# Performance work log

Hardware: AMD Instinct MI355X
Metric: run time of the kernel (lower is better)

Reference implementation:

```python
import jax, jax.numpy as jnp
import numpy as np

N, E, IN, H, OUT = 50000, 800000, 128, 128, 64
BN_EPS = 1e-5


def setup_inputs() -> dict:
    key = jax.random.key(0)
    ks = jax.random.split(key, 12)
    x = jax.random.normal(ks[0], (N, IN), dtype=jnp.float32)
    edge_index = jax.random.randint(ks[1], (2, E), 0, N, dtype=jnp.int32)
    def lin(k, fan_in, fan_out):
        s = 1.0 / np.sqrt(fan_in)
        return jax.random.uniform(k, (fan_in, fan_out), jnp.float32, -s, s)
    params = {
        'W1': lin(ks[2], IN, H),  'b1': jnp.zeros((H,), jnp.float32),
        'W2': lin(ks[3], H, H),   'b2': jnp.zeros((H,), jnp.float32),
        'W3': lin(ks[4], H, H),   'b3': jnp.zeros((H,), jnp.float32),
        'W4': lin(ks[5], H, OUT), 'b4': jnp.zeros((OUT,), jnp.float32),
        'g1': jnp.ones((H,), jnp.float32), 'be1': jnp.zeros((H,), jnp.float32),
        'g2': jnp.ones((H,), jnp.float32), 'be2': jnp.zeros((H,), jnp.float32),
        'g3': jnp.ones((H,), jnp.float32), 'be3': jnp.zeros((H,), jnp.float32),
    }
    return dict(x=x, edge_index=edge_index, **params)


def _gcn_conv(x, src, dst, dinv, norm, W, b):
    # GCNConv: symmetric-normalized aggregation with self loops.
    h = x @ W                                   # [N, F]
    agg = jax.ops.segment_sum(h[src] * norm[:, None], dst, num_segments=N)
    agg = agg + h * (dinv * dinv)[:, None]      # self-loop contribution
    return agg + b


def _bn(x, gamma, beta):
    mu = jnp.mean(x, axis=0)
    var = jnp.mean(jnp.square(x - mu), axis=0)
    return (x - mu) * jax.lax.rsqrt(var + BN_EPS) * gamma + beta


def reference(x, edge_index, W1, b1, W2, b2, W3, b3, W4, b4, g1, be1, g2, be2, g3, be3):
    src, dst = edge_index[0], edge_index[1]
    # degree with self loops; fixed by the graph, shared across layers
    deg = jax.ops.segment_sum(jnp.ones((E,), x.dtype), dst, num_segments=N) + 1.0
    dinv = jax.lax.rsqrt(deg)
    norm = dinv[src] * dinv[dst]                # [E]

    h = _gcn_conv(x, src, dst, dinv, norm, W1, b1)
    h = jax.nn.relu(_bn(h, g1, be1))
    h = _gcn_conv(h, src, dst, dinv, norm, W2, b2)
    h = jax.nn.relu(_bn(h, g2, be2))
    h = _gcn_conv(h, src, dst, dinv, norm, W3, b3)
    h = jax.nn.relu(_bn(h, g3, be3))
    return _gcn_conv(h, src, dst, dinv, norm, W4, b4)
```

## Files before the change

kernel.cpp:

```cpp
#include <hip/hip_runtime.h>

constexpr int NN = 50000;
constexpr int NE = 800000;
constexpr float EPS = 1e-5f;

constexpr int CAP     = 64;
constexpr int FILL_NB = (NE + 255) / 256;
constexpr int WCONV_NB = (57344 + 255) / 256;
constexpr int GEMM1_NB = (NN + 63) / 64;

constexpr int GROUPS   = 197;
constexpr int FUSED_NB = GROUPS * 21;

typedef short bf16x8 __attribute__((ext_vector_type(8)));
typedef float f32x4  __attribute__((ext_vector_type(4)));

__device__ __forceinline__ ushort f2bf(float x) {
    union { float f; unsigned u; } a; a.f = x;
    unsigned u = a.u;
    unsigned r = (u + 0x7FFFu + ((u >> 16) & 1u)) >> 16;
    return (ushort)r;
}
__device__ __forceinline__ float bflo(unsigned p) {
    union { unsigned u; float f; } a; a.u = p << 16; return a.f;
}
__device__ __forceinline__ float bfhi(unsigned p) {
    union { unsigned u; float f; } a; a.u = p & 0xFFFF0000u; return a.f;
}

__global__ __launch_bounds__(256, 3) void fused_prep_gemm1(
    const int* __restrict__ src, const int* __restrict__ dst,
    int* __restrict__ curA, int* __restrict__ curB,
    ushort* __restrict__ csrf,
    const float* __restrict__ W1, const float* __restrict__ W2,
    const float* __restrict__ W3, const float* __restrict__ W4,
    ushort* __restrict__ Wt,
    const float* __restrict__ X, ushort* __restrict__ U)
{
    constexpr int LDK = 136;
    __shared__ __align__(16) ushort Xs[64 * LDK];

    const int bx  = blockIdx.x;
    const int g   = bx / 21;
    const int l   = bx - g * 21;
    const int tid = threadIdx.x;

    if (l >= 4) {
        int fid = g * 17 + (l - 4);
        if (fid < FILL_NB) {
            int e = fid * 256 + tid;
            if (e < NE) {
                int d = dst[e];
                if (e < NE / 2) {
                    int slot = atomicAdd(&curA[d], 1);
                    if (slot < CAP) csrf[(size_t)d * CAP + slot] = (ushort)src[e];
                } else {
                    int old = atomicAdd(&curB[d], 1);
                    int slot = CAP - 1 - old;
                    if (slot >= 0) csrf[(size_t)d * CAP + slot] = (ushort)src[e];
                }
            }
        } else {
            int id = (fid - FILL_NB) * 256 + tid;
            if (id < 49152) {
                int li = id / 16384, r = id % 16384;
                int n = r >> 7, k = r & 127;
                const float* W = (li == 0) ? W1 : (li == 1) ? W2 : W3;
                Wt[li * 16384 + n * 128 + k] = f2bf(W[k * 128 + n]);
            } else if (id < 57344) {
                int r = id - 49152;
                int n = r >> 7, k = r & 127;
                Wt[49152 + n * 128 + k] = f2bf(W4[k * 64 + n]);
            }
        }
        return;
    }

    int tile = g * 4 + l;
    if (tile >= GEMM1_NB) return;

    const int wave = tid >> 6;
    const int lane = tid & 63;
    const int m    = lane & 15;
    const int q    = lane >> 4;
    const int rowHalf = wave & 1;
    const int colHalf = wave >> 1;
    const int row0 = tile * 64;

    bf16x8 w[4][4];
#pragma unroll
    for (int nt = 0; nt < 4; nt++) {
#pragma unroll
        for (int ks = 0; ks < 4; ks++) {
            const float* wp = &W1[(ks * 32 + q * 8) * 128 + colHalf * 64 + nt * 16 + m];
            bf16x8 t;
#pragma unroll
            for (int j = 0; j < 8; j++) t[j] = (short)f2bf(wp[j * 128]);
            w[nt][ks] = t;
        }
    }

#pragma unroll
    for (int it = 0; it < 8; it++) {
        int idx = it * 256 + tid;
        int r   = idx >> 5;
        int c4  = (idx & 31) * 4;
        int row = row0 + r;
        float4 v = make_float4(0.f, 0.f, 0.f, 0.f);
        if (row < NN) v = *(const float4*)&X[(size_t)row * 128 + c4];
        ushort4 o;
        o.x = f2bf(v.x); o.y = f2bf(v.y); o.z = f2bf(v.z); o.w = f2bf(v.w);
        *(ushort4*)&Xs[r * LDK + c4] = o;
    }
    __syncthreads();

    f32x4 acc[2][4];
#pragma unroll
    for (int t = 0; t < 2; t++)
#pragma unroll
        for (int nt = 0; nt < 4; nt++) acc[t][nt] = (f32x4){0.f, 0.f, 0.f, 0.f};

#pragma unroll
    for (int ks = 0; ks < 4; ks++) {
        bf16x8 a0 = *(const bf16x8*)&Xs[(rowHalf * 32 + m)      * LDK + ks * 32 + q * 8];
        bf16x8 a1 = *(const bf16x8*)&Xs[(rowHalf * 32 + 16 + m) * LDK + ks * 32 + q * 8];
#pragma unroll
        for (int nt = 0; nt < 4; nt++) {
            acc[0][nt] = __builtin_amdgcn_mfma_f32_16x16x32_bf16(a0, w[nt][ks], acc[0][nt], 0, 0, 0);
            acc[1][nt] = __builtin_amdgcn_mfma_f32_16x16x32_bf16(a1, w[nt][ks], acc[1][nt], 0, 0, 0);
        }
    }

#pragma unroll
    for (int t = 0; t < 2; t++) {
#pragma unroll
        for (int r = 0; r < 4; r++) {
            int row = row0 + rowHalf * 32 + t * 16 + q * 4 + r;
            if (row < NN) {
#pragma unroll
                for (int nt = 0; nt < 4; nt++)
                    U[(size_t)row * 128 + colHalf * 64 + nt * 16 + m] = f2bf(acc[t][nt][r]);
            }
        }
    }
}

template<int F, bool BN>
__global__ __launch_bounds__(256, 3) void gemm_bf16_kernel(
    const void* __restrict__ Xv, const ushort* __restrict__ Wt,
    const int* __restrict__ curA, const int* __restrict__ curB,
    const float* __restrict__ sums, const float* __restrict__ sumsq,
    const float* __restrict__ g, const float* __restrict__ be,
    ushort* __restrict__ U)
{
    constexpr int NTW = F / 32;
    constexpr int LDK = 136;
    __shared__ __align__(16) ushort Xs[64 * LDK];
    __shared__ float scs[128], shs[128];

    const int tid  = threadIdx.x;
    const int wave = tid >> 6;
    const int lane = tid & 63;
    const int m    = lane & 15;
    const int q    = lane >> 4;
    const int rowHalf = wave & 1;
    const int colHalf = wave >> 1;
    const int row0 = blockIdx.x * 64;

    if constexpr (BN) {
        if (tid < 128) {
            float mu  = sums[tid] * (1.0f / NN);
            float var = sumsq[tid] * (1.0f / NN) - mu * mu;
            float scv = rsqrtf(var + EPS) * g[tid];
            scs[tid] = scv;
            shs[tid] = be[tid] - mu * scv;
        }
        __syncthreads();
    }

    bf16x8 w[NTW][4];
#pragma unroll
    for (int nt = 0; nt < NTW; nt++)
#pragma unroll
        for (int ks = 0; ks < 4; ks++)
            w[nt][ks] = *(const bf16x8*)&Wt[(colHalf * (F / 2) + nt * 16 + m) * 128 + ks * 32 + q * 8];

#pragma unroll
    for (int it = 0; it < 8; it++) {
        int idx = it * 256 + tid;
        int r   = idx >> 5;
        int c4  = (idx & 31) * 4;
        int row = row0 + r;
        float4 v = make_float4(0.f, 0.f, 0.f, 0.f);
        if constexpr (BN) {
            if (row < NN) {
                uint2 p = *(const uint2*)&((const ushort*)Xv)[(size_t)row * 128 + c4];
                v.x = bflo(p.x); v.y = bfhi(p.x);
                v.z = bflo(p.y); v.w = bfhi(p.y);
            }
            float4 s = *(const float4*)&scs[c4];
            float4 h = *(const float4*)&shs[c4];
            v.x = fmaxf(0.f, v.x * s.x + h.x);
            v.y = fmaxf(0.f, v.y * s.y + h.y);
            v.z = fmaxf(0.f, v.z * s.z + h.z);
            v.w = fmaxf(0.f, v.w * s.w + h.w);
        } else {
            if (row < NN) v = *(const float4*)&((const float*)Xv)[(size_t)row * 128 + c4];
        }
        ushort4 o;
        o.x = f2bf(v.x); o.y = f2bf(v.y); o.z = f2bf(v.z); o.w = f2bf(v.w);
        *(ushort4*)&Xs[r * LDK + c4] = o;
    }
    __syncthreads();

    f32x4 acc[2][NTW];
#pragma unroll
    for (int t = 0; t < 2; t++)
#pragma unroll
        for (int nt = 0; nt < NTW; nt++) acc[t][nt] = (f32x4){0.f, 0.f, 0.f, 0.f};

#pragma unroll
    for (int ks = 0; ks < 4; ks++) {
        bf16x8 a0 = *(const bf16x8*)&Xs[(rowHalf * 32 + m)      * LDK + ks * 32 + q * 8];
        bf16x8 a1 = *(const bf16x8*)&Xs[(rowHalf * 32 + 16 + m) * LDK + ks * 32 + q * 8];
#pragma unroll
        for (int nt = 0; nt < NTW; nt++) {
            acc[0][nt] = __builtin_amdgcn_mfma_f32_16x16x32_bf16(a0, w[nt][ks], acc[0][nt], 0, 0, 0);
            acc[1][nt] = __builtin_amdgcn_mfma_f32_16x16x32_bf16(a1, w[nt][ks], acc[1][nt], 0, 0, 0);
        }
    }

#pragma unroll
    for (int t = 0; t < 2; t++) {
#pragma unroll
        for (int r = 0; r < 4; r++) {
            int row = row0 + rowHalf * 32 + t * 16 + q * 4 + r;
            if (row < NN) {
                float di = rsqrtf((float)(curA[row] + curB[row]) + 1.0f);
#pragma unroll
                for (int nt = 0; nt < NTW; nt++) {
                    U[(size_t)row * F + colHalf * (F / 2) + nt * 16 + m] = f2bf(acc[t][nt][r] * di);
                }
            }
        }
    }
}

template<bool SRCSCALE>
__global__ __launch_bounds__(256) void gather128_kernel(
    const ushort* __restrict__ csrf,
    const int* __restrict__ curA, const int* __restrict__ curB,
    const ushort* __restrict__ U, const float* __restrict__ b,
    ushort* __restrict__ Yb)
{
    int n    = (blockIdx.x * 256 + threadIdx.x) >> 6;
    int lane = threadIdx.x & 63;
    if (n >= NN) return;
    const int half = lane >> 5;
    const int c4   = (lane & 31) * 4;
    int dA = curA[n], dB = curB[n];
    int degRaw = dA + dB;
    int dA_c = min(dA, CAP);
    int dB_c = min(dB, CAP - dA_c);
    const int cnt = dA_c + dB_c;
    const int gap = CAP - cnt;
    int myIdx = (int)csrf[(size_t)n * CAP + lane];
    float myDs = 0.f;
    if constexpr (SRCSCALE) {
        int mi = min(myIdx, NN - 1);
        myDs = rsqrtf((float)(curA[mi] + curB[mi]) + 1.0f);
    }
    float a0 = 0.f, a1 = 0.f, a2 = 0.f, a3 = 0.f;

#define GSLOT(v) ((v) < dA_c ? (v) : (v) + gap)

    int j = 0;
    for (; j + 16 <= cnt; j += 16) {
        int s0 = __shfl(myIdx, GSLOT(j + 0  + half));
        int s1 = __shfl(myIdx, GSLOT(j + 2  + half));
        int s2 = __shfl(myIdx, GSLOT(j + 4  + half));
        int s3 = __shfl(myIdx, GSLOT(j + 6  + half));
        int s4 = __shfl(myIdx, GSLOT(j + 8  + half));
        int s5 = __shfl(myIdx, GSLOT(j + 10 + half));
        int s6 = __shfl(myIdx, GSLOT(j + 12 + half));
        int s7 = __shfl(myIdx, GSLOT(j + 14 + half));
        uint2 u0 = *(const uint2*)&U[(size_t)s0 * 128 + c4];
        uint2 u1 = *(const uint2*)&U[(size_t)s1 * 128 + c4];
        uint2 u2 = *(const uint2*)&U[(size_t)s2 * 128 + c4];
        uint2 u3 = *(const uint2*)&U[(size_t)s3 * 128 + c4];
        uint2 u4 = *(const uint2*)&U[(size_t)s4 * 128 + c4];
        uint2 u5 = *(const uint2*)&U[(size_t)s5 * 128 + c4];
        uint2 u6 = *(const uint2*)&U[(size_t)s6 * 128 + c4];
        uint2 u7 = *(const uint2*)&U[(size_t)s7 * 128 + c4];
        if constexpr (SRCSCALE) {
            float c0 = __shfl(myDs, GSLOT(j + 0  + half));
            float c1 = __shfl(myDs, GSLOT(j + 2  + half));
            float c2 = __shfl(myDs, GSLOT(j + 4  + half));
            float c3 = __shfl(myDs, GSLOT(j + 6  + half));
            float c5 = __shfl(myDs, GSLOT(j + 10 + half));
            float c4s = __shfl(myDs, GSLOT(j + 8 + half));
            float c6 = __shfl(myDs, GSLOT(j + 12 + half));
            float c7 = __shfl(myDs, GSLOT(j + 14 + half));
            a0 += c0 * bflo(u0.x) + c1 * bflo(u1.x) + c2 * bflo(u2.x) + c3 * bflo(u3.x)
                + c4s * bflo(u4.x) + c5 * bflo(u5.x) + c6 * bflo(u6.x) + c7 * bflo(u7.x);
            a1 += c0 * bfhi(u0.x) + c1 * bfhi(u1.x) + c2 * bfhi(u2.x) + c3 * bfhi(u3.x)
                + c4s * bfhi(u4.x) + c5 * bfhi(u5.x) + c6 * bfhi(u6.x) + c7 * bfhi(u7.x);
            a2 += c0 * bflo(u0.y) + c1 * bflo(u1.y) + c2 * bflo(u2.y) + c3 * bflo(u3.y)
                + c4s * bflo(u4.y) + c5 * bflo(u5.y) + c6 * bflo(u6.y) + c7 * bflo(u7.y);
            a3 += c0 * bfhi(u0.y) + c1 * bfhi(u1.y) + c2 * bfhi(u2.y) + c3 * bfhi(u3.y)
                + c4s * bfhi(u4.y) + c5 * bfhi(u5.y) + c6 * bfhi(u6.y) + c7 * bfhi(u7.y);
        } else {
            a0 += bflo(u0.x) + bflo(u1.x) + bflo(u2.x) + bflo(u3.x)
                + bflo(u4.x) + bflo(u5.x) + bflo(u6.x) + bflo(u7.x);
            a1 += bfhi(u0.x) + bfhi(u1.x) + bfhi(u2.x) + bfhi(u3.x)
                + bfhi(u4.x) + bfhi(u5.x) + bfhi(u6.x) + bfhi(u7.x);
            a2 += bflo(u0.y) + bflo(u1.y) + bflo(u2.y) + bflo(u3.y)
                + bflo(u4.y) + bflo(u5.y) + bflo(u6.y) + bflo(u7.y);
            a3 += bfhi(u0.y) + bfhi(u1.y) + bfhi(u2.y) + bfhi(u3.y)
                + bfhi(u4.y) + bfhi(u5.y) + bfhi(u6.y) + bfhi(u7.y);
        }
    }
    for (; j + 8 <= cnt; j += 8) {
        int s0 = __shfl(myIdx, GSLOT(j + 0 + half));
        int s1 = __shfl(myIdx, GSLOT(j + 2 + half));
        int s2 = __shfl(myIdx, GSLOT(j + 4 + half));
        int s3 = __shfl(myIdx, GSLOT(j + 6 + half));
        uint2 u0 = *(const uint2*)&U[(size_t)s0 * 128 + c4];
        uint2 u1 = *(const uint2*)&U[(size_t)s1 * 128 + c4];
        uint2 u2 = *(const uint2*)&U[(size_t)s2 * 128 + c4];
        uint2 u3 = *(const uint2*)&U[(size_t)s3 * 128 + c4];
        if constexpr (SRCSCALE) {
            float c0 = __shfl(myDs, GSLOT(j + 0 + half));
            float c1 = __shfl(myDs, GSLOT(j + 2 + half));
            float c2 = __shfl(myDs, GSLOT(j + 4 + half));
            float c3 = __shfl(myDs, GSLOT(j + 6 + half));
            a0 += c0 * bflo(u0.x) + c1 * bflo(u1.x) + c2 * bflo(u2.x) + c3 * bflo(u3.x);
            a1 += c0 * bfhi(u0.x) + c1 * bfhi(u1.x) + c2 * bfhi(u2.x) + c3 * bfhi(u3.x);
            a2 += c0 * bflo(u0.y) + c1 * bflo(u1.y) + c2 * bflo(u2.y) + c3 * bflo(u3.y);
            a3 += c0 * bfhi(u0.y) + c1 * bfhi(u1.y) + c2 * bfhi(u2.y) + c3 * bfhi(u3.y);
        } else {
            a0 += bflo(u0.x) + bflo(u1.x) + bflo(u2.x) + bflo(u3.x);
            a1 += bfhi(u0.x) + bfhi(u1.x) + bfhi(u2.x) + bfhi(u3.x);
            a2 += bflo(u0.y) + bflo(u1.y) + bflo(u2.y) + bflo(u3.y);
            a3 += bfhi(u0.y) + bfhi(u1.y) + bfhi(u2.y) + bfhi(u3.y);
        }
    }
    for (; j + 4 <= cnt; j += 4) {
        int s0 = __shfl(myIdx, GSLOT(j + 0 + half));
        int s1 = __shfl(myIdx, GSLOT(j + 2 + half));
        uint2 u0 = *(const uint2*)&U[(size_t)s0 * 128 + c4];
        uint2 u1 = *(const uint2*)&U[(size_t)s1 * 128 + c4];
        if constexpr (SRCSCALE) {
            float c0 = __shfl(myDs, GSLOT(j + 0 + half));
            float c1 = __shfl(myDs, GSLOT(j + 2 + half));
            a0 += c0 * bflo(u0.x) + c1 * bflo(u1.x);
            a1 += c0 * bfhi(u0.x) + c1 * bfhi(u1.x);
            a2 += c0 * bflo(u0.y) + c1 * bflo(u1.y);
            a3 += c0 * bfhi(u0.y) + c1 * bfhi(u1.y);
        } else {
            a0 += bflo(u0.x) + bflo(u1.x);
            a1 += bfhi(u0.x) + bfhi(u1.x);
            a2 += bflo(u0.y) + bflo(u1.y);
            a3 += bfhi(u0.y) + bfhi(u1.y);
        }
    }
    for (; j < cnt; j += 2) {
        int jj = j + half;
        int vv = min(jj, cnt - 1);
        int sl = GSLOT(vv);
        int s  = __shfl(myIdx, sl);
        float sc = 1.f;
        if constexpr (SRCSCALE) sc = __shfl(myDs, sl);
        uint2 u = *(const uint2*)&U[(size_t)s * 128 + c4];
        if (jj < cnt) {
            a0 += sc * bflo(u.x); a1 += sc * bfhi(u.x);
            a2 += sc * bflo(u.y); a3 += sc * bfhi(u.y);
        }
    }
#undef GSLOT

    a0 += __shfl_xor(a0, 32);
    a1 += __shfl_xor(a1, 32);
    a2 += __shfl_xor(a2, 32);
    a3 += __shfl_xor(a3, 32);

    uint2 us = *(const uint2*)&U[(size_t)n * 128 + c4];
    float di = rsqrtf((float)degRaw + 1.0f);
    float selfs = SRCSCALE ? di : 1.0f;
    float4 bb = *(const float4*)&b[c4];
    float o0 = di * (a0 + selfs * bflo(us.x)) + bb.x;
    float o1 = di * (a1 + selfs * bfhi(us.x)) + bb.y;
    float o2 = di * (a2 + selfs * bflo(us.y)) + bb.z;
    float o3 = di * (a3 + selfs * bfhi(us.y)) + bb.w;
    if (half == 0) {
        ushort4 o;
        o.x = f2bf(o0); o.y = f2bf(o1); o.z = f2bf(o2); o.w = f2bf(o3);
        *(ushort4*)&Yb[(size_t)n * 128 + c4] = o;
    }
}

__global__ __launch_bounds__(256) void gather64_kernel(
    const ushort* __restrict__ csrf,
    const int* __restrict__ curA, const int* __restrict__ curB,
    const ushort* __restrict__ U, const float* __restrict__ b,
    float* __restrict__ Y)
{
    int t  = blockIdx.x * 256 + threadIdx.x;
    int n  = t >> 5;
    int l2 = t & 31;
    if (n >= NN) return;
    const int coff = l2 * 2;
    int dA = curA[n], dB = curB[n];
    int degRaw = dA + dB;
    int dA_c = min(dA, CAP);
    int dB_c = min(dB, CAP - dA_c);
    const int cnt = dA_c + dB_c;
    const int gap = CAP - cnt;
    int iA = (int)csrf[(size_t)n * CAP + l2];
    int iB = (int)csrf[(size_t)n * CAP + 32 + l2];
    float ax = 0.f, ay = 0.f;

#define GIDX(v, sv)                                            \
    int sv;                                                    \
    {                                                          \
        int _s = ((v) < dA_c) ? (v) : (v) + gap;               \
        int _l = __shfl(iA, _s & 31, 32);                      \
        int _h = __shfl(iB, _s & 31, 32);                      \
        sv = (_s < 32) ? _l : _h;                              \
    }

    int j = 0;
    for (; j + 8 <= cnt; j += 8) {
        GIDX(j + 0, s0) GIDX(j + 1, s1) GIDX(j + 2, s2) GIDX(j + 3, s3)
        GIDX(j + 4, s4) GIDX(j + 5, s5) GIDX(j + 6, s6) GIDX(j + 7, s7)
        unsigned u0 = *(const unsigned*)&U[(size_t)s0 * 64 + coff];
        unsigned u1 = *(const unsigned*)&U[(size_t)s1 * 64 + coff];
        unsigned u2 = *(const unsigned*)&U[(size_t)s2 * 64 + coff];
        unsigned u3 = *(const unsigned*)&U[(size_t)s3 * 64 + coff];
        unsigned u4 = *(const unsigned*)&U[(size_t)s4 * 64 + coff];
        unsigned u5 = *(const unsigned*)&U[(size_t)s5 * 64 + coff];
        unsigned u6 = *(const unsigned*)&U[(size_t)s6 * 64 + coff];
        unsigned u7 = *(const unsigned*)&U[(size_t)s7 * 64 + coff];
        ax += bflo(u0) + bflo(u1) + bflo(u2) + bflo(u3)
            + bflo(u4) + bflo(u5) + bflo(u6) + bflo(u7);
        ay += bfhi(u0) + bfhi(u1) + bfhi(u2) + bfhi(u3)
            + bfhi(u4) + bfhi(u5) + bfhi(u6) + bfhi(u7);
    }
    for (; j + 4 <= cnt; j += 4) {
        GIDX(j + 0, s0) GIDX(j + 1, s1) GIDX(j + 2, s2) GIDX(j + 3, s3)
        unsigned u0 = *(const unsigned*)&U[(size_t)s0 * 64 + coff];
        unsigned u1 = *(const unsigned*)&U[(size_t)s1 * 64 + coff];
        unsigned u2 = *(const unsigned*)&U[(size_t)s2 * 64 + coff];
        unsigned u3 = *(const unsigned*)&U[(size_t)s3 * 64 + coff];
        ax += bflo(u0) + bflo(u1) + bflo(u2) + bflo(u3);
        ay += bfhi(u0) + bfhi(u1) + bfhi(u2) + bfhi(u3);
    }
    for (; j < cnt; j++) {
        GIDX(j, s)
        unsigned u = *(const unsigned*)&U[(size_t)s * 64 + coff];
        ax += bflo(u); ay += bfhi(u);
    }
#undef GIDX

    unsigned us = *(const unsigned*)&U[(size_t)n * 64 + coff];
    float di = rsqrtf((float)degRaw + 1.0f);
    float ox = di * (ax + bflo(us)) + b[coff];
    float oy = di * (ay + bfhi(us)) + b[coff + 1];
    *(float2*)&Y[(size_t)n * 64 + coff] = make_float2(ox, oy);
}

__global__ __launch_bounds__(256) void stats_kernel(const ushort* __restrict__ Yb,
                                                    float* __restrict__ sums,
                                                    float* __restrict__ sumsq)
{
    __shared__ float ssum[128], ssq[128];
    if (threadIdx.x < 128) { ssum[threadIdx.x] = 0.f; ssq[threadIdx.x] = 0.f; }
    __syncthreads();

    const int lane   = threadIdx.x & 63;
    const int gwave  = (blockIdx.x * 256 + threadIdx.x) >> 6;
    const int nWaves = gridDim.x * 4;
    const int coff   = lane * 2;

    float s0 = 0.f, s1 = 0.f, q0 = 0.f, q1 = 0.f;
    for (int row = gwave; row < NN; row += nWaves) {
        unsigned p = *(const unsigned*)&Yb[(size_t)row * 128 + coff];
        float yx = bflo(p), yy = bfhi(p);
        s0 += yx; q0 += yx * yx;
        s1 += yy; q1 += yy * yy;
    }
    atomicAdd(&ssum[coff], s0);     atomicAdd(&ssum[coff + 1], s1);
    atomicAdd(&ssq[coff], q0);      atomicAdd(&ssq[coff + 1], q1);
    __syncthreads();
    if (threadIdx.x < 128) {
        atomicAdd(&sums[threadIdx.x],  ssum[threadIdx.x]);
        atomicAdd(&sumsq[threadIdx.x], ssq[threadIdx.x]);
    }
}

extern "C" void kernel_launch(void* const* d_in, const int* in_sizes, int n_in,
                              void* d_out, int out_size, void* d_ws, size_t ws_size,
                              hipStream_t stream)
{
    const float* x   = (const float*)d_in[0];
    const int*   ei  = (const int*)d_in[1];
    const int*   src = ei;
    const int*   dst = ei + NE;
    const float* W1 = (const float*)d_in[2];  const float* b1 = (const float*)d_in[3];
    const float* W2 = (const float*)d_in[4];  const float* b2 = (const float*)d_in[5];
    const float* W3 = (const float*)d_in[6];  const float* b3 = (const float*)d_in[7];
    const float* W4 = (const float*)d_in[8];  const float* b4 = (const float*)d_in[9];
    const float* g1 = (const float*)d_in[10]; const float* be1 = (const float*)d_in[11];
    const float* g2 = (const float*)d_in[12]; const float* be2 = (const float*)d_in[13];
    const float* g3 = (const float*)d_in[14]; const float* be3 = (const float*)d_in[15];
    float* out = (float*)d_out;

    char* wsb = (char*)d_ws;
    int*   curA   = (int*)wsb;
    int*   curB   = curA + NN;
    float* stats  = (float*)(curB + NN);
    ushort* Wt    = (ushort*)(stats + 768);
    ushort* csrf  = Wt + 57344;
    ushort* Yb    = csrf + (size_t)NN * CAP;
    ushort* U     = Yb + (size_t)NN * 128;

    float* sums1 = stats;       float* sumsq1 = stats + 128;
    float* sums2 = stats + 256; float* sumsq2 = stats + 384;
    float* sums3 = stats + 512; float* sumsq3 = stats + 640;

    const ushort* Wt2 = Wt + 16384;
    const ushort* Wt3 = Wt + 32768;
    const ushort* Wt4 = Wt + 49152;

    const int gemmGrid   = (NN + 63) / 64;
    const int gathGrid   = (NN * 64 + 255) / 256;
    const int gath64Grid = (NN * 32 + 255) / 256;

    hipMemsetAsync(curA, 0, 2 * NN * sizeof(int) + 768 * sizeof(float), stream);
    fused_prep_gemm1<<<FUSED_NB, 256, 0, stream>>>(src, dst, curA, curB, csrf,
                                                   W1, W2, W3, W4, Wt, x, U);

    gather128_kernel<true><<<gathGrid, 256, 0, stream>>>(csrf, curA, curB, U, b1, Yb);
    stats_kernel<<<512, 256, 0, stream>>>(Yb, sums1, sumsq1);

    gemm_bf16_kernel<128, true><<<gemmGrid, 256, 0, stream>>>(Yb, Wt2, curA, curB, sums1, sumsq1, g1, be1, U);
    gather128_kernel<false><<<gathGrid, 256, 0, stream>>>(csrf, curA, curB, U, b2, Yb);
    stats_kernel<<<512, 256, 0, stream>>>(Yb, sums2, sumsq2);

    gemm_bf16_kernel<128, true><<<gemmGrid, 256, 0, stream>>>(Yb, Wt3, curA, curB, sums2, sumsq2, g2, be2, U);
    gather128_kernel<false><<<gathGrid, 256, 0, stream>>>(csrf, curA, curB, U, b3, Yb);
    stats_kernel<<<512, 256, 0, stream>>>(Yb, sums3, sumsq3);

    gemm_bf16_kernel<64, true><<<gemmGrid, 256, 0, stream>>>(Yb, Wt4, curA, curB, sums3, sumsq3, g3, be3, U);
    gather64_kernel<<<gath64Grid, 256, 0, stream>>>(csrf, curA, curB, U, b4, out);
}
```

Measured before the change: 366.0 us.

## Partition CSR fill by destination range across blocks sharing edge chunks

The edge-to-CSR fill is restructured. Each block now scans a 2048-edge chunk but only inserts edges whose destination falls in one of eight node ranges, so eight blocks cooperate on each chunk. The aim is to localize atomics and CSR writes to a destination slice, likely for better cache locality across XCDs. The grouping of GEMM1 tiles and weight-conversion blocks changes to match. The cost is that dst is read eight times over, and each block does more serial work.

```diff
diff --git a/kernel.cpp b/kernel.cpp
--- a/kernel.cpp
+++ b/kernel.cpp
@@ -5,12 +5,15 @@
 constexpr float EPS = 1e-5f;
 
 constexpr int CAP     = 64;
-constexpr int FILL_NB = (NE + 255) / 256;
 constexpr int WCONV_NB = (57344 + 255) / 256;
 constexpr int GEMM1_NB = (NN + 63) / 64;
 
-constexpr int GROUPS   = 197;
-constexpr int FUSED_NB = GROUPS * 21;
+constexpr int GROUPS   = 98;
+constexpr int GSIZE    = 48;
+constexpr int FUSED_NB = GROUPS * GSIZE;
+constexpr int ECHUNK   = 2048;
+constexpr int NCHUNK   = (NE + ECHUNK - 1) / ECHUNK;
+constexpr int DSTR     = NN / 8;
 
 typedef short bf16x8 __attribute__((ext_vector_type(8)));
 typedef float f32x4  __attribute__((ext_vector_type(4)));
@@ -41,42 +44,54 @@
     __shared__ __align__(16) ushort Xs[64 * LDK];
 
     const int bx  = blockIdx.x;
-    const int g   = bx / 21;
-    const int l   = bx - g * 21;
+    const int g   = bx / GSIZE;
+    const int l   = bx - g * GSIZE;
     const int tid = threadIdx.x;
 
-    if (l >= 4) {
-        int fid = g * 17 + (l - 4);
-        if (fid < FILL_NB) {
-            int e = fid * 256 + tid;
-            if (e < NE) {
-                int d = dst[e];
-                if (e < NE / 2) {
-                    int slot = atomicAdd(&curA[d], 1);
-                    if (slot < CAP) csrf[(size_t)d * CAP + slot] = (ushort)src[e];
-                } else {
-                    int old = atomicAdd(&curB[d], 1);
-                    int slot = CAP - 1 - old;
-                    if (slot >= 0) csrf[(size_t)d * CAP + slot] = (ushort)src[e];
+    if (l >= 8) {
+        const int c    = l & 7;
+        const int rank = (l - 8) >> 3;
+        const int cid  = g + GROUPS * rank;
+        if (cid < NCHUNK) {
+            const int lo = c * DSTR, hi = lo + DSTR;
+            const int base = cid * ECHUNK;
+#pragma unroll
+            for (int i = 0; i < ECHUNK / 256; i++) {
+                int e = base + i * 256 + tid;
+                if (e < NE) {
+                    int d = dst[e];
+                    if (d >= lo && d < hi) {
+                        if (e < NE / 2) {
+                            int slot = atomicAdd(&curA[d], 1);
+                            if (slot < CAP) csrf[(size_t)d * CAP + slot] = (ushort)src[e];
+                        } else {
+                            int old = atomicAdd(&curB[d], 1);
+                            int slot = CAP - 1 - old;
+                            if (slot >= 0) csrf[(size_t)d * CAP + slot] = (ushort)src[e];
+                        }
+                    }
                 }
             }
         } else {
-            int id = (fid - FILL_NB) * 256 + tid;
-            if (id < 49152) {
-                int li = id / 16384, r = id % 16384;
-                int n = r >> 7, k = r & 127;
-                const float* W = (li == 0) ? W1 : (li == 1) ? W2 : W3;
-                Wt[li * 16384 + n * 128 + k] = f2bf(W[k * 128 + n]);
-            } else if (id < 57344) {
-                int r = id - 49152;
-                int n = r >> 7, k = r & 127;
-                Wt[49152 + n * 128 + k] = f2bf(W4[k * 64 + n]);
+            int wid = (cid - NCHUNK) * 8 + c;
+            if (wid < WCONV_NB) {
+                int id = wid * 256 + tid;
+                if (id < 49152) {
+                    int li = id / 16384, r = id % 16384;
+                    int n = r >> 7, k = r & 127;
+                    const float* W = (li == 0) ? W1 : (li == 1) ? W2 : W3;
+                    Wt[li * 16384 + n * 128 + k] = f2bf(W[k * 128 + n]);
+                } else if (id < 57344) {
+                    int r = id - 49152;
+                    int n = r >> 7, k = r & 127;
+                    Wt[49152 + n * 128 + k] = f2bf(W4[k * 64 + n]);
+                }
             }
         }
         return;
     }
 
-    int tile = g * 4 + l;
+    int tile = g * 8 + l;
     if (tile >= GEMM1_NB) return;
 
     const int wave = tid >> 6;
```

After: 378.0 us. 1.03x slower.
